# Kernel tuning notes

Measured on AMD Instinct MI355X. Metric: run time of the kernel, lower is better.

Reference implementation:

```python
import jax, jax.numpy as jnp
import numpy as np

B, Cin, Cout, H, W = 4, 256, 256, 64, 64
DG, KH, KW = 2, 3, 3        # deformable_groups=2, kernel 3x3
K = KH * KW
CG = Cin // DG


def setup_inputs() -> dict:
    key = jax.random.key(0)
    ks = jax.random.split(key, 4)
    x = jax.random.normal(ks[0], (B, Cin, H, W), jnp.float32)
    # offset/mask-predicting 3x3 conv: 3*DG*K = 54 output channels
    # (small weights so sampled offsets stay in a realistic +-few-pixel range)
    w_off = jax.random.normal(ks[1], (3 * DG * K, Cin, KH, KW), jnp.float32) * 0.01
    b_off = jnp.zeros((3 * DG * K,), jnp.float32)
    weight = jax.random.normal(ks[2], (Cout, Cin, KH, KW), jnp.float32) * (1.0 / np.sqrt(Cin * K))
    bias = jnp.zeros((Cout,), jnp.float32)
    return {"x": x, "w_off": w_off, "b_off": b_off, "weight": weight, "bias": bias}


def _dcn_forward(x, w_off, b_off, weight, bias):
    # 1) predict offsets + modulation mask with a regular 3x3 conv
    om = jax.lax.conv_general_dilated(
        x, w_off, window_strides=(1, 1), padding=((1, 1), (1, 1)),
        dimension_numbers=('NCHW', 'OIHW', 'NCHW'))
    om = om + b_off[None, :, None, None]
    off = om[:, :2 * DG * K].reshape(B, DG, 2, K, H, W)        # [.,.,(dy,dx),k,h,w]
    mask = jax.nn.sigmoid(om[:, 2 * DG * K:]).reshape(B, DG, K, H, W)

    # 2) sampling positions: base grid (stride 1, pad 1, dilation 1) + learned offsets
    ky = jnp.repeat(jnp.arange(KH), KW).astype(jnp.float32)    # [K]
    kx = jnp.tile(jnp.arange(KW), KH).astype(jnp.float32)
    gy = jnp.arange(H, dtype=jnp.float32)
    gx = jnp.arange(W, dtype=jnp.float32)
    py = off[:, :, 0] + (gy[None, None, None, :, None] + ky[None, None, :, None, None] - 1.0)  # [B,DG,K,H,W]
    px = off[:, :, 1] + (gx[None, None, None, None, :] + kx[None, None, :, None, None] - 1.0)

    y0 = jnp.floor(py); x0 = jnp.floor(px)
    wy1 = py - y0; wx1 = px - x0
    wy0 = 1.0 - wy1; wx0 = 1.0 - wx1
    y0i = y0.astype(jnp.int32); x0i = x0.astype(jnp.int32)

    imgf = x.reshape(B, DG, CG, H * W)  # channel groups share their group's offsets

    def gather(iy, ix):
        # zero padding outside the image, as in the DCNv2 CUDA kernel
        valid = ((iy >= 0) & (iy < H) & (ix >= 0) & (ix < W)).astype(x.dtype)  # [B,DG,K,H,W]
        idx = jnp.clip(iy, 0, H - 1) * W + jnp.clip(ix, 0, W - 1)
        idx = idx.reshape(B, DG, K * H * W)
        v = jax.vmap(jax.vmap(lambda im, ii: im[:, ii]))(imgf, idx)  # [B,DG,CG,K*H*W]
        return v.reshape(B, DG, CG, K, H, W) * valid[:, :, None]

    # 3) bilinear interpolation of the 4 corners
    sampled = (gather(y0i,     x0i)     * (wy0 * wx0)[:, :, None]
             + gather(y0i,     x0i + 1) * (wy0 * wx1)[:, :, None]
             + gather(y0i + 1, x0i)     * (wy1 * wx0)[:, :, None]
             + gather(y0i + 1, x0i + 1) * (wy1 * wx1)[:, :, None])
    sampled = sampled * mask[:, :, None]  # modulation (DCNv2)

    # 4) weighted accumulation == grouped contraction over (channel, tap)
    wr = weight.reshape(Cout, DG, CG, K)
    out = jnp.einsum('odck,bdckhw->bohw', wr, sampled) + bias[None, :, None, None]
    return out


def reference(x, w_off, b_off, weight, bias):
    return _dcn_forward(x, w_off, b_off, weight, bias)
```

## Files before the change

### kernel.cpp

```cpp
#include <hip/hip_runtime.h>
#include <cstdint>

#define HW 4096

typedef __attribute__((ext_vector_type(8))) short bf16x8;
typedef __attribute__((ext_vector_type(4))) float f32x4;

__device__ __forceinline__ short f2bf(float f) {
    union { float f; uint32_t u; } v; v.f = f;
    uint32_t u = v.u;
    uint32_t r = (u + 0x7FFFu + ((u >> 16) & 1u)) >> 16;
    return (short)(r & 0xFFFFu);
}
__device__ __forceinline__ uint32_t cvtpk(float lo, float hi) {
    uint32_t r;
    asm("v_cvt_pk_bf16_f32 %0, %1, %2" : "=v"(r) : "v"(lo), "v"(hi));
    return r;
}
__device__ __forceinline__ float blo(uint32_t u) { return __uint_as_float(u << 16); }
__device__ __forceinline__ float bhi(uint32_t u) { return __uint_as_float(u & 0xFFFF0000u); }
__device__ __forceinline__ void glds16(const void* g, void* l) {
    __builtin_amdgcn_global_load_lds(
        (const __attribute__((address_space(1))) void*)g,
        (__attribute__((address_space(3))) void*)l, 16, 0, 0);
}

__global__ __launch_bounds__(256) void k_xt(
    const float* __restrict__ x, unsigned short* __restrict__ xT)
{
    __shared__ unsigned short s[64][65];
    const int t = threadIdx.x, lane = t & 63, grp = t >> 6;
    const int hw0 = blockIdx.x * 64, c0 = blockIdx.y * 64, b = blockIdx.z;
#pragma unroll
    for (int j = 0; j < 16; ++j) {
        int cc = grp * 16 + j;
        float v = x[((size_t)(b * 256 + c0 + cc)) * HW + hw0 + lane];
        s[cc][lane] = (unsigned short)f2bf(v);
    }
    __syncthreads();
#pragma unroll
    for (int j = 0; j < 16; ++j) {
        int hw2 = grp * 16 + j;
        xT[((size_t)b * HW + hw0 + hw2) * 256 + c0 + lane] = s[lane][hw2];
    }
}

__global__ __launch_bounds__(256) void k_wcvt_all(
    const float* __restrict__ weight, const float* __restrict__ w_off,
    short* __restrict__ a2, short* __restrict__ wTb)
{
    int e = blockIdx.x * 256 + threadIdx.x;
    if (e < 589824) {
        int o = e / 2304, r = e - o * 2304;
        int dg = r / 1152, r2 = r - dg * 1152;
        int tap = r2 >> 7, c = r2 & 127;
        a2[e] = f2bf(weight[o * 2304 + (dg * 128 + c) * 9 + tap]);
    } else {
        int e2 = e - 589824;
        int o = e2 / 2304, r = e2 - o * 2304;
        int tap = r >> 8, c = r & 255;
        wTb[e2] = (o < 54) ? f2bf(w_off[(o * 256 + c) * 9 + tap]) : (short)0;
    }
}

__global__ __launch_bounds__(256, 4) void k_omgemm(
    const short* __restrict__ wTb, const unsigned short* __restrict__ xT,
    float* __restrict__ om2p)
{
    __shared__ short As[2][64 * 32];
    __shared__ short Bs[2][64 * 32];
    const int t = threadIdx.x;
    const int wid = __builtin_amdgcn_readfirstlane(t >> 6);
    const int lane = t & 63, quad = lane >> 4, l16 = lane & 15;
    const int n0 = blockIdx.x * 64, b = n0 >> 12;
    const int ks = blockIdx.y;
    const int nr = t >> 2;
    const int ksh = (t & 3) * 8;
    const int px = (n0 + nr) & 4095, h = px >> 6, w = px & 63;
    const unsigned short* xb = xT + (size_t)b * HW * 256;
    const int cbase = ks * 18;

    auto loadB = [&](int c) -> uint4 {
        int tap = c >> 3, c0 = (c & 7) * 32;
        int hh = h + tap / 3 - 1, ww = w + tap % 3 - 1;
        uint4 bv = {0u, 0u, 0u, 0u};
        if (hh >= 0 && hh < 64 && ww >= 0 && ww < 64)
            bv = *(const uint4*)(xb + (size_t)(hh * 64 + ww) * 256 + c0 + ksh);
        return bv;
    };

    f32x4 acc[4];
#pragma unroll
    for (int i = 0; i < 4; ++i) acc[i] = (f32x4){0.f, 0.f, 0.f, 0.f};

    uint4 bv[2];
    bv[0] = loadB(cbase);
    glds16(wTb + (size_t)nr * 2304 + cbase * 32 + ksh, &As[0][t * 8]);
    *(uint4*)&Bs[0][t * 8] = bv[0];
    bv[1] = loadB(cbase + 1);

#pragma unroll 2
    for (int i = 0; i < 18; ++i) {
        const int p = i & 1;
        __syncthreads();
        if (i < 17) {
            glds16(wTb + (size_t)nr * 2304 + (cbase + i + 1) * 32 + ksh,
                   &As[1 - p][t * 8]);
            *(uint4*)&Bs[1 - p][t * 8] = bv[(i + 1) & 1];
        }
        if (i + 2 < 18) bv[i & 1] = loadB(cbase + i + 2);
        bf16x8 bf = *(const bf16x8*)&Bs[p][(wid * 16 + l16) * 32 + quad * 8];
#pragma unroll
        for (int mi = 0; mi < 4; ++mi) {
            bf16x8 af = *(const bf16x8*)&As[p][(mi * 16 + l16) * 32 + quad * 8];
            acc[mi] = __builtin_amdgcn_mfma_f32_16x16x32_bf16(af, bf, acc[mi], 0, 0, 0);
        }
    }
    const int n = n0 + wid * 16 + l16;
#pragma unroll
    for (int mi = 0; mi < 4; ++mi)
#pragma unroll
        for (int i = 0; i < 4; ++i)
            om2p[(size_t)(ks * 64 + mi * 16 + quad * 4 + i) * 16384 + n] = acc[mi][i];
}

__global__ __launch_bounds__(256) void k_plan(
    const float* __restrict__ om2p, const float* __restrict__ b_off,
    float4* __restrict__ planw, int4* __restrict__ plani)
{
    int e = blockIdx.x * 256 + threadIdx.x;
    int n = e & 16383, s = e >> 14;
    int dg = s >= 9 ? 1 : 0, tap = s - dg * 9;
    int h = (n >> 6) & 63, w = n & 63;
    int cdy = dg * 18 + tap, cdx = cdy + 9, cms = 36 + dg * 9 + tap;
    float dy = b_off[cdy], dx = b_off[cdx], ms = b_off[cms];
#pragma unroll
    for (int cs = 0; cs < 4; ++cs) {
        const float* p = om2p + (size_t)cs * 64 * 16384;
        dy += p[(size_t)cdy * 16384 + n];
        dx += p[(size_t)cdx * 16384 + n];
        ms += p[(size_t)cms * 16384 + n];
    }
    ms = 1.f / (1.f + __expf(-ms));
    float py = dy + (float)(h + tap / 3 - 1);
    float qx = dx + (float)(w + tap % 3 - 1);
    float y0f = floorf(py), x0f = floorf(qx);
    float wy1 = py - y0f, wx1 = qx - x0f;
    float wy0 = 1.f - wy1, wx0 = 1.f - wx1;
    int y0 = (int)y0f, x0 = (int)x0f;
    int y1 = y0 + 1, x1 = x0 + 1;
    bool vy0 = (y0 >= 0) & (y0 < 64), vy1 = (y1 >= 0) & (y1 < 64);
    bool vx0 = (x0 >= 0) & (x0 < 64), vx1 = (x1 >= 0) & (x1 < 64);
    int cy0 = min(max(y0, 0), 63), cy1 = min(max(y1, 0), 63);
    int cx0 = min(max(x0, 0), 63), cx1 = min(max(x1, 0), 63);
    float4 wv;
    wv.x = (vy0 && vx0) ? wy0 * wx0 * ms : 0.f;
    wv.y = (vy0 && vx1) ? wy0 * wx1 * ms : 0.f;
    wv.z = (vy1 && vx0) ? wy1 * wx0 * ms : 0.f;
    wv.w = (vy1 && vx1) ? wy1 * wx1 * ms : 0.f;
    int4 iv = make_int4((cy0 * 64 + cx0) << 9, (cy0 * 64 + cx1) << 9,
                        (cy1 * 64 + cx0) << 9, (cy1 * 64 + cx1) << 9);
    planw[e] = wv;
    plani[e] = iv;
}

__global__ __launch_bounds__(1024, 4) void k_fused(
    const short* __restrict__ A, const unsigned short* __restrict__ xT,
    const float4* __restrict__ planw, const int4* __restrict__ plani,
    const float* __restrict__ bias, float* __restrict__ out)
{
    __shared__ short As[2][4][256 * 32];
    __shared__ short Bs[2][4][64 * 32];
    const int t = threadIdx.x;
    const int wid = __builtin_amdgcn_readfirstlane(t >> 6);
    const int lane = t & 63;
    const int quad = lane >> 4, l16 = lane & 15;
    const int wr = wid & 7, wc = wid >> 3;

    const int lin = blockIdx.x;
    const int bn = ((lin & 7) << 5) | (lin >> 3);

    const int n0 = bn * 64, b = n0 >> 12;
    const char* xbb = (const char*)xT + (size_t)b * HW * 512;
    const int px = t >> 4;
    const int cc = (t >> 2) & 3;
    const int q8 = (t & 3) * 8;
    const int n = n0 + px;

    f32x4 acc[2][2];
#pragma unroll
    for (int i = 0; i < 2; ++i)
#pragma unroll
        for (int j = 0; j < 2; ++j) acc[i][j] = (f32x4){0.f, 0.f, 0.f, 0.f};

    float4 pw[2];
    int4 pi[2];
    uint4 g[2][4];

    auto pwload = [&](int S) { pw[S & 1] = planw[(size_t)S * 16384 + n]; };
    auto piload = [&](int S) { pi[S & 1] = plani[(size_t)S * 16384 + n]; };
    auto gather = [&](int j, uint4* gd) {
        const int cb = ((j >= 9 ? 128 : 0) + cc * 32 + q8) * 2;
        const int4 i4 = pi[j & 1];
        gd[0] = *(const uint4*)(xbb + i4.x + cb);
        gd[1] = *(const uint4*)(xbb + i4.y + cb);
        gd[2] = *(const uint4*)(xbb + i4.z + cb);
        gd[3] = *(const uint4*)(xbb + i4.w + cb);
    };
    const int arow = t >> 2;
    const int aq = t & 3;
    const int asw = (aq ^ ((arow >> 1) & 3)) * 8;
    auto stageA = [&](int j, int buf) {
#pragma unroll
        for (int ss = 0; ss < 4; ++ss)
            glds16(A + (size_t)arow * 2304 + (4 * j + ss) * 32 + asw,
                   &As[buf][ss][arow * 32 + aq * 8]);
    };
    const int bsw = ((t & 3) ^ ((px >> 1) & 3)) * 8;
    auto packwrite = [&](int j, int buf) {
        const float4 w4 = pw[j & 1];
        const uint4* gd = g[j & 1];
        float a0 = w4.x * blo(gd[0].x) + w4.y * blo(gd[1].x) + w4.z * blo(gd[2].x) + w4.w * blo(gd[3].x);
        float a1 = w4.x * bhi(gd[0].x) + w4.y * bhi(gd[1].x) + w4.z * bhi(gd[2].x) + w4.w * bhi(gd[3].x);
        float a2v = w4.x * blo(gd[0].y) + w4.y * blo(gd[1].y) + w4.z * blo(gd[2].y) + w4.w * blo(gd[3].y);
        float a3 = w4.x * bhi(gd[0].y) + w4.y * bhi(gd[1].y) + w4.z * bhi(gd[2].y) + w4.w * bhi(gd[3].y);
        float a4 = w4.x * blo(gd[0].z) + w4.y * blo(gd[1].z) + w4.z * blo(gd[2].z) + w4.w * blo(gd[3].z);
        float a5 = w4.x * bhi(gd[0].z) + w4.y * bhi(gd[1].z) + w4.z * bhi(gd[2].z) + w4.w * bhi(gd[3].z);
        float a6 = w4.x * blo(gd[0].w) + w4.y * blo(gd[1].w) + w4.z * blo(gd[2].w) + w4.w * blo(gd[3].w);
        float a7 = w4.x * bhi(gd[0].w) + w4.y * bhi(gd[1].w) + w4.z * bhi(gd[2].w) + w4.w * bhi(gd[3].w);
        uint4 o;
        o.x = cvtpk(a0, a1); o.y = cvtpk(a2v, a3);
        o.z = cvtpk(a4, a5); o.w = cvtpk(a6, a7);
        *(uint4*)&Bs[buf][cc][px * 32 + bsw] = o;
    };

    pwload(0);
    piload(0);
    gather(0, g[0]);
    stageA(0, 0);
    __builtin_amdgcn_sched_barrier(0);
    packwrite(0, 0);
    pwload(1);
    piload(1);
    piload(2);
    gather(1, g[1]);

#pragma unroll 2
    for (int i = 0; i < 18; ++i) {
        const int p = i & 1;
        __builtin_amdgcn_sched_barrier(0);
        if (i < 17)
            asm volatile("s_waitcnt vmcnt(4) lgkmcnt(0)" ::: "memory");
        else
            asm volatile("s_waitcnt vmcnt(0) lgkmcnt(0)" ::: "memory");
        __builtin_amdgcn_s_barrier();
        __builtin_amdgcn_sched_barrier(0);
        if (i < 17) {
            stageA(i + 1, 1 - p);
            __builtin_amdgcn_sched_barrier(0);
            packwrite(i + 1, 1 - p);
        }
        if (i + 2 < 18) pwload(i + 2);
        if (i + 3 < 18) piload(i + 3);
        if (i + 2 < 18) gather(i + 2, g[i & 1]);
#pragma unroll
        for (int ss = 0; ss < 4; ++ss) {
            bf16x8 bfr[2];
#pragma unroll
            for (int ni = 0; ni < 2; ++ni) {
                const int row = wc * 32 + ni * 16 + l16;
                bfr[ni] = *(const bf16x8*)&Bs[p][ss][row * 32 + (quad ^ ((row >> 1) & 3)) * 8];
            }
#pragma unroll
            for (int mi = 0; mi < 2; ++mi) {
                const int row = wr * 32 + mi * 16 + l16;
                bf16x8 af = *(const bf16x8*)&As[p][ss][row * 32 + (quad ^ ((row >> 1) & 3)) * 8];
#pragma unroll
                for (int ni = 0; ni < 2; ++ni)
                    acc[mi][ni] = __builtin_amdgcn_mfma_f32_16x16x32_bf16(
                        af, bfr[ni], acc[mi][ni], 0, 0, 0);
            }
        }
    }

    const int m0 = wr * 32;
#pragma unroll
    for (int mi = 0; mi < 2; ++mi)
#pragma unroll
        for (int ni = 0; ni < 2; ++ni) {
            int nn = n0 + wc * 32 + ni * 16 + l16;
            int bidx = nn >> 12, hw = nn & 4095;
            float* op = out + (size_t)bidx * 256 * 4096 + hw;
#pragma unroll
            for (int r = 0; r < 4; ++r) {
                int m = m0 + mi * 16 + quad * 4 + r;
                op[(size_t)m * 4096] = acc[mi][ni][r] + bias[m];
            }
        }
}

extern "C" void kernel_launch(void* const* d_in, const int* in_sizes, int n_in,
                              void* d_out, int out_size, void* d_ws, size_t ws_size,
                              hipStream_t stream)
{
    const float* x      = (const float*)d_in[0];
    const float* w_off  = (const float*)d_in[1];
    const float* b_off  = (const float*)d_in[2];
    const float* weight = (const float*)d_in[3];
    const float* bias   = (const float*)d_in[4];
    float* out = (float*)d_out;
    char* ws = (char*)d_ws;

    unsigned short* xT   = (unsigned short*)(ws);
    short*          a2   = (short*)(ws + 8388608);
    short*          wTb  = (short*)(ws + 9568256);
    float4*         planw= (float4*)(ws + 9863168);
    int4*           plani= (int4*)(ws + 14581760);
    float*          om2p = (float*)d_out;

    hipLaunchKernelGGL(k_xt, dim3(64, 4, 4), dim3(256), 0, stream, x, xT);
    hipLaunchKernelGGL(k_wcvt_all, dim3(2880), dim3(256), 0, stream,
                       weight, w_off, a2, wTb);
    hipLaunchKernelGGL(k_omgemm, dim3(256, 4), dim3(256), 0, stream, wTb, xT, om2p);
    hipLaunchKernelGGL(k_plan, dim3(1152), dim3(256), 0, stream, om2p, b_off, planw, plani);
    hipLaunchKernelGGL(k_fused, dim3(256), dim3(1024), 0, stream,
                       a2, xT, planw, plani, bias, out);
}
```

Before: 142.3 us.

## Load weight fragments directly into registers in MFMA layout instead of LDS staging

The weight conversion kernel now writes the bf16 weight matrix pre-swizzled into the per-lane MFMA A-fragment order. The fused DCN kernel loads those fragments straight from global memory into registers, which removes the shared-memory A tile and its global-to-LDS staging. The pipeline is also simplified: one gather buffer, a plain __syncthreads in place of the hand-tuned waitcnt/barrier schedule, and packwrite moved after the MFMAs. The aim is to cut LDS traffic and LDS footprint. The cost is that every wave re-reads weights from global/L2 each step, and the gather prefetch now runs only one step ahead, so less latency is hidden.

```diff
diff --git a/kernel.cpp b/kernel.cpp
--- a/kernel.cpp
+++ b/kernel.cpp
@@ -47,14 +47,19 @@
 
 __global__ __launch_bounds__(256) void k_wcvt_all(
     const float* __restrict__ weight, const float* __restrict__ w_off,
-    short* __restrict__ a2, short* __restrict__ wTb)
+    short* __restrict__ a2r, short* __restrict__ wTb)
 {
     int e = blockIdx.x * 256 + threadIdx.x;
     if (e < 589824) {
-        int o = e / 2304, r = e - o * 2304;
-        int dg = r / 1152, r2 = r - dg * 1152;
-        int tap = r2 >> 7, c = r2 & 127;
-        a2[e] = f2bf(weight[o * 2304 + (dg * 128 + c) * 9 + tap]);
+        int el = e & 7;
+        int lane = (e >> 3) & 63;
+        int rg = (e >> 9) & 15;
+        int ss = (e >> 13) & 3;
+        int j = e >> 15;
+        int o = rg * 16 + (lane & 15);
+        int cch = ss * 32 + (lane >> 4) * 8 + el;
+        int dg = j / 9, tap = j - dg * 9;
+        a2r[e] = f2bf(weight[o * 2304 + (dg * 128 + cch) * 9 + tap]);
     } else {
         int e2 = e - 589824;
         int o = e2 / 2304, r = e2 - o * 2304;
@@ -165,11 +170,10 @@
 }
 
 __global__ __launch_bounds__(1024, 4) void k_fused(
-    const short* __restrict__ A, const unsigned short* __restrict__ xT,
+    const short* __restrict__ A2r, const unsigned short* __restrict__ xT,
     const float4* __restrict__ planw, const int4* __restrict__ plani,
     const float* __restrict__ bias, float* __restrict__ out)
 {
-    __shared__ short As[2][4][256 * 32];
     __shared__ short Bs[2][4][64 * 32];
     const int t = threadIdx.x;
     const int wid = __builtin_amdgcn_readfirstlane(t >> 6);
@@ -187,6 +191,8 @@
     const int q8 = (t & 3) * 8;
     const int n = n0 + px;
 
+    const short* Aw = A2r + (size_t)(wr * 2) * 512 + lane * 8;
+
     f32x4 acc[2][2];
 #pragma unroll
     for (int i = 0; i < 2; ++i)
@@ -195,39 +201,37 @@
 
     float4 pw[2];
     int4 pi[2];
-    uint4 g[2][4];
+    uint4 g[4];
 
     auto pwload = [&](int S) { pw[S & 1] = planw[(size_t)S * 16384 + n]; };
     auto piload = [&](int S) { pi[S & 1] = plani[(size_t)S * 16384 + n]; };
-    auto gather = [&](int j, uint4* gd) {
+    auto gather = [&](int j) {
         const int cb = ((j >= 9 ? 128 : 0) + cc * 32 + q8) * 2;
         const int4 i4 = pi[j & 1];
-        gd[0] = *(const uint4*)(xbb + i4.x + cb);
-        gd[1] = *(const uint4*)(xbb + i4.y + cb);
-        gd[2] = *(const uint4*)(xbb + i4.z + cb);
-        gd[3] = *(const uint4*)(xbb + i4.w + cb);
+        g[0] = *(const uint4*)(xbb + i4.x + cb);
+        g[1] = *(const uint4*)(xbb + i4.y + cb);
+        g[2] = *(const uint4*)(xbb + i4.z + cb);
+        g[3] = *(const uint4*)(xbb + i4.w + cb);
     };
-    const int arow = t >> 2;
-    const int aq = t & 3;
-    const int asw = (aq ^ ((arow >> 1) & 3)) * 8;
-    auto stageA = [&](int j, int buf) {
+    auto aload = [&](int j, uint4* ar) {
 #pragma unroll
         for (int ss = 0; ss < 4; ++ss)
-            glds16(A + (size_t)arow * 2304 + (4 * j + ss) * 32 + asw,
-                   &As[buf][ss][arow * 32 + aq * 8]);
+#pragma unroll
+            for (int mi = 0; mi < 2; ++mi)
+                ar[ss * 2 + mi] =
+                    *(const uint4*)(Aw + (size_t)(j * 4 + ss) * 8192 + mi * 512);
     };
     const int bsw = ((t & 3) ^ ((px >> 1) & 3)) * 8;
     auto packwrite = [&](int j, int buf) {
         const float4 w4 = pw[j & 1];
-        const uint4* gd = g[j & 1];
-        float a0 = w4.x * blo(gd[0].x) + w4.y * blo(gd[1].x) + w4.z * blo(gd[2].x) + w4.w * blo(gd[3].x);
-        float a1 = w4.x * bhi(gd[0].x) + w4.y * bhi(gd[1].x) + w4.z * bhi(gd[2].x) + w4.w * bhi(gd[3].x);
-        float a2v = w4.x * blo(gd[0].y) + w4.y * blo(gd[1].y) + w4.z * blo(gd[2].y) + w4.w * blo(gd[3].y);
-        float a3 = w4.x * bhi(gd[0].y) + w4.y * bhi(gd[1].y) + w4.z * bhi(gd[2].y) + w4.w * bhi(gd[3].y);
-        float a4 = w4.x * blo(gd[0].z) + w4.y * blo(gd[1].z) + w4.z * blo(gd[2].z) + w4.w * blo(gd[3].z);
-        float a5 = w4.x * bhi(gd[0].z) + w4.y * bhi(gd[1].z) + w4.z * bhi(gd[2].z) + w4.w * bhi(gd[3].z);
-        float a6 = w4.x * blo(gd[0].w) + w4.y * blo(gd[1].w) + w4.z * blo(gd[2].w) + w4.w * blo(gd[3].w);
-        float a7 = w4.x * bhi(gd[0].w) + w4.y * bhi(gd[1].w) + w4.z * bhi(gd[2].w) + w4.w * bhi(gd[3].w);
+        float a0 = w4.x * blo(g[0].x) + w4.y * blo(g[1].x) + w4.z * blo(g[2].x) + w4.w * blo(g[3].x);
+        float a1 = w4.x * bhi(g[0].x) + w4.y * bhi(g[1].x) + w4.z * bhi(g[2].x) + w4.w * bhi(g[3].x);
+        float a2v = w4.x * blo(g[0].y) + w4.y * blo(g[1].y) + w4.z * blo(g[2].y) + w4.w * blo(g[3].y);
+        float a3 = w4.x * bhi(g[0].y) + w4.y * bhi(g[1].y) + w4.z * bhi(g[2].y) + w4.w * bhi(g[3].y);
+        float a4 = w4.x * blo(g[0].z) + w4.y * blo(g[1].z) + w4.z * blo(g[2].z) + w4.w * blo(g[3].z);
+        float a5 = w4.x * bhi(g[0].z) + w4.y * bhi(g[1].z) + w4.z * bhi(g[2].z) + w4.w * bhi(g[3].z);
+        float a6 = w4.x * blo(g[0].w) + w4.y * blo(g[1].w) + w4.z * blo(g[2].w) + w4.w * blo(g[3].w);
+        float a7 = w4.x * bhi(g[0].w) + w4.y * bhi(g[1].w) + w4.z * bhi(g[2].w) + w4.w * bhi(g[3].w);
         uint4 o;
         o.x = cvtpk(a0, a1); o.y = cvtpk(a2v, a3);
         o.z = cvtpk(a4, a5); o.w = cvtpk(a6, a7);
@@ -236,33 +240,20 @@
 
     pwload(0);
     piload(0);
-    gather(0, g[0]);
-    stageA(0, 0);
-    __builtin_amdgcn_sched_barrier(0);
+    gather(0);
     packwrite(0, 0);
     pwload(1);
     piload(1);
-    piload(2);
-    gather(1, g[1]);
 
 #pragma unroll 2
     for (int i = 0; i < 18; ++i) {
         const int p = i & 1;
+        __syncthreads();
+        uint4 ar[8];
+        aload(i, ar);
+        if (i + 1 < 18) gather(i + 1);
+        if (i + 2 < 18) { pwload(i + 2); piload(i + 2); }
         __builtin_amdgcn_sched_barrier(0);
-        if (i < 17)
-            asm volatile("s_waitcnt vmcnt(4) lgkmcnt(0)" ::: "memory");
-        else
-            asm volatile("s_waitcnt vmcnt(0) lgkmcnt(0)" ::: "memory");
-        __builtin_amdgcn_s_barrier();
-        __builtin_amdgcn_sched_barrier(0);
-        if (i < 17) {
-            stageA(i + 1, 1 - p);
-            __builtin_amdgcn_sched_barrier(0);
-            packwrite(i + 1, 1 - p);
-        }
-        if (i + 2 < 18) pwload(i + 2);
-        if (i + 3 < 18) piload(i + 3);
-        if (i + 2 < 18) gather(i + 2, g[i & 1]);
 #pragma unroll
         for (int ss = 0; ss < 4; ++ss) {
             bf16x8 bfr[2];
@@ -273,14 +264,14 @@
             }
 #pragma unroll
             for (int mi = 0; mi < 2; ++mi) {
-                const int row = wr * 32 + mi * 16 + l16;
-                bf16x8 af = *(const bf16x8*)&As[p][ss][row * 32 + (quad ^ ((row >> 1) & 3)) * 8];
+                bf16x8 af = *(const bf16x8*)&ar[ss * 2 + mi];
 #pragma unroll
                 for (int ni = 0; ni < 2; ++ni)
                     acc[mi][ni] = __builtin_amdgcn_mfma_f32_16x16x32_bf16(
                         af, bfr[ni], acc[mi][ni], 0, 0, 0);
             }
         }
+        if (i + 1 < 18) packwrite(i + 1, 1 - p);
     }
 
     const int m0 = wr * 32;
@@ -312,7 +303,7 @@
     char* ws = (char*)d_ws;
 
     unsigned short* xT   = (unsigned short*)(ws);
-    short*          a2   = (short*)(ws + 8388608);
+    short*          a2r  = (short*)(ws + 8388608);
     short*          wTb  = (short*)(ws + 9568256);
     float4*         planw= (float4*)(ws + 9863168);
     int4*           plani= (int4*)(ws + 14581760);
@@ -320,9 +311,9 @@
 
     hipLaunchKernelGGL(k_xt, dim3(64, 4, 4), dim3(256), 0, stream, x, xT);
     hipLaunchKernelGGL(k_wcvt_all, dim3(2880), dim3(256), 0, stream,
-                       weight, w_off, a2, wTb);
+                       weight, w_off, a2r, wTb);
     hipLaunchKernelGGL(k_omgemm, dim3(256, 4), dim3(256), 0, stream, wTb, xT, om2p);
     hipLaunchKernelGGL(k_plan, dim3(1152), dim3(256), 0, stream, om2p, b_off, planw, plani);
     hipLaunchKernelGGL(k_fused, dim3(256), dim3(1024), 0, stream,
-                       a2, xT, planw, plani, bias, out);
-}
+                       a2r, xT, planw, plani, bias, out);
+}
```

Result: slower. 147.2 us (+3.4%).
